# Kernel tuning notes

Measured on AMD Instinct MI355X. Metric: run time of the kernel, lower is better.

Reference implementation:

```python
import jax, jax.numpy as jnp
import numpy as np
from jax import lax


def _sobel3d_kernels():
    # Standard separable 3D Sobel: derivative d=[-1,0,1] along one axis,
    # smoothing s=[1,2,1] along the other two. Axes order (D, H, W).
    d = np.array([-1.0, 0.0, 1.0], dtype=np.float32)
    s = np.array([1.0, 2.0, 1.0], dtype=np.float32)
    kx = np.einsum('i,j,k->ijk', d, s, s)  # derivative along D
    ky = np.einsum('i,j,k->ijk', s, d, s)  # derivative along H
    kz = np.einsum('i,j,k->ijk', s, s, d)  # derivative along W
    # Stack as [Cout=3, Cin=1, 3, 3, 3] -> one conv computes x,y,z grads at once.
    return jnp.asarray(np.stack([kx, ky, kz])[:, None])


_DN = ('NCDHW', 'OIDHW', 'NCDHW')


def _conv3(x, k):
    # x: [N, 1, D, H, W], k: [3, 1, 3, 3, 3] -> [N, 3, D-2, H-2, W-2]
    # torch F.conv3d and lax conv are both cross-correlation; VALID padding.
    return lax.conv_general_dilated(x, k, (1, 1, 1), 'VALID', dimension_numbers=_DN)


def _g2(inp, k):
    # inp: [B, D, H, W, C] (channels last, as the torch module permutes)
    b, dd, hh, ww, c = inp.shape
    x = jnp.transpose(inp, (0, 4, 1, 2, 3)).reshape(b * c, 1, dd, hh, ww)
    g1 = _conv3(x, k)                                  # [B*C, 3, D-2, H-2, W-2]
    mag = jnp.sqrt(jnp.sum(g1 * g1, axis=1, keepdims=True))  # first-order magnitude
    g2 = _conv3(mag, k)                                # [B*C, 3, D-4, H-4, W-4]
    gx, gy, gz = g2[:, 0], g2[:, 1], g2[:, 2]
    # Faithful to source: sqrt(x^2 + y^2) + z^2 (note: z is squared, not inside sqrt)
    out = jnp.sqrt(gx * gx + gy * gy) + gz * gz        # [B*C, D-4, H-4, W-4]
    return out.reshape(b, c, *out.shape[1:])


def setup_inputs() -> dict:
    key = jax.random.key(0)
    k1, k2 = jax.random.split(key)
    pred = jax.random.normal(k1, (2, 64, 64, 64, 32), dtype=jnp.float32)
    hr = jax.random.normal(k2, (2, 64, 64, 64, 32), dtype=jnp.float32)
    return {'pred': pred, 'hr': hr}


def reference(pred, hr):
    k = _sobel3d_kernels()
    return jnp.mean(jnp.abs(_g2(pred, k) - _g2(hr, k)))
```

## Files before the change

kernel.cpp:

```cpp
#include <hip/hip_runtime.h>
#include <hip/hip_fp16.h>


constexpr int BDIM = 256;
constexpr size_t IN_B = 8388608;
constexpr int IN_D = 131072;
constexpr int IN_H = 2048;
constexpr int M = 62;
constexpr int F = 60;
constexpr int C = 32;
constexpr int MROW = M * C;
constexpr size_t MAGSZ = (size_t)M * M * MROW;
constexpr size_t PLANE = (size_t)M * MROW;
constexpr unsigned NPART = 1440;

__device__ __forceinline__ float4 ld4(const float* p) {
    return *reinterpret_cast<const float4*>(p);
}
__device__ __forceinline__ float4 ldh4(const __half* p) {
    float2 r = *reinterpret_cast<const float2*>(p);
    const __half2* h = reinterpret_cast<const __half2*>(&r);
    float2 lo = __half22float2(h[0]), hi = __half22float2(h[1]);
    return make_float4(lo.x, lo.y, hi.x, hi.y);
}
__device__ __forceinline__ float4 sm3(float4 a, float4 b, float4 c) {
    return make_float4(a.x + 2.f * b.x + c.x, a.y + 2.f * b.y + c.y,
                       a.z + 2.f * b.z + c.z, a.w + 2.f * b.w + c.w);
}
__device__ __forceinline__ float4 df2(float4 a, float4 c) {
    return make_float4(c.x - a.x, c.y - a.y, c.z - a.z, c.w - a.w);
}

struct P1W { float4 A[2], B[2], C[2]; };

__device__ __forceinline__ void p1_plane(const float* __restrict__ col, size_t zoff,
                                         P1W& W)
{
    float4 S[4], D[4];
#pragma unroll
    for (int r = 0; r < 4; ++r) {
        const float* p = col + zoff + (size_t)r * IN_H;
        float4 a = ld4(p), b = ld4(p + C), c = ld4(p + 2 * C);
        S[r] = sm3(a, b, c);
        D[r] = df2(a, c);
    }
#pragma unroll
    for (int k = 0; k < 2; ++k) {
        W.A[k] = sm3(S[k], S[k+1], S[k+2]);
        W.B[k] = df2(S[k], S[k+2]);
        W.C[k] = sm3(D[k], D[k+1], D[k+2]);
    }
}

__device__ __forceinline__ void p1_emit(const P1W& W0, const P1W& W1, const P1W& W2,
                                        __half* __restrict__ mag, size_t cb,
                                        int z, int y0, bool wr)
{
    if (!wr) return;
#pragma unroll
    for (int k = 0; k < 2; ++k) {
        float4 gx = df2(W0.A[k], W2.A[k]);
        float4 gy = sm3(W0.B[k], W1.B[k], W2.B[k]);
        float4 gz = sm3(W0.C[k], W1.C[k], W2.C[k]);
        float m0 = sqrtf(gx.x * gx.x + gy.x * gy.x + gz.x * gz.x);
        float m1 = sqrtf(gx.y * gx.y + gy.y * gy.y + gz.y * gz.y);
        float m2 = sqrtf(gx.z * gx.z + gy.z * gy.z + gz.z * gz.z);
        float m3 = sqrtf(gx.w * gx.w + gy.w * gy.w + gz.w * gz.w);
        union { __half2 h[2]; float2 f; } u;
        u.h[0] = __floats2half2_rn(m0, m1);
        u.h[1] = __floats2half2_rn(m2, m3);
        *reinterpret_cast<float2*>(mag + ((size_t)z * M + (y0 + k)) * MROW + cb)
            = u.f;
    }
}

__device__ __forceinline__ void p1_unit(const float* __restrict__ in,
                                        __half* __restrict__ mag,
                                        int b, int bx, int zc, int tid)
{
    const int xt = bx & 1, yt = bx >> 1;
    const int c4 = (tid & 7) << 2;
    const int xl = tid >> 3;
    const int x  = xt * 30 + xl;
    const bool wr = (xt == 0) || (xl >= 2);
    const int y0 = yt * 2;
    const int z0 = zc * 8;
    const int zn = min(8, M - z0);

    const float* col = in + (size_t)b * IN_B + (size_t)y0 * IN_H
                          + (size_t)x * C + c4;
    const size_t cb = (size_t)x * C + c4;

    P1W W0, W1, W2;
    p1_plane(col, (size_t)(z0 + 0) * IN_D, W0);
    p1_plane(col, (size_t)(z0 + 1) * IN_D, W1);
    int z = 0;
    while (true) {
        p1_plane(col, (size_t)(z0 + z + 2) * IN_D, W2);
        p1_emit(W0, W1, W2, mag, cb, z0 + z, y0, wr);
        if (++z >= zn) break;
        p1_plane(col, (size_t)(z0 + z + 2) * IN_D, W0);
        p1_emit(W1, W2, W0, mag, cb, z0 + z, y0, wr);
        if (++z >= zn) break;
        p1_plane(col, (size_t)(z0 + z + 2) * IN_D, W1);
        p1_emit(W2, W0, W1, mag, cb, z0 + z, y0, wr);
        if (++z >= zn) break;
    }
}

__global__ __launch_bounds__(BDIM) void sobel_mag_v10(
    const float* __restrict__ pred, const float* __restrict__ hr,
    __half* __restrict__ magP, __half* __restrict__ magH,
    int b, unsigned* __restrict__ counter, int zeroCtr)
{
    if (zeroCtr && blockIdx.x == 0 && blockIdx.y == 0 && blockIdx.z == 0 &&
        threadIdx.x == 0)
        __hip_atomic_store(counter, 0u, __ATOMIC_RELAXED,
                           __HIP_MEMORY_SCOPE_AGENT);
    const float* in = blockIdx.z ? hr : pred;
    __half* mag = blockIdx.z ? magH : magP;
    p1_unit(in, mag, b, blockIdx.x, blockIdx.y, threadIdx.x);
}

struct P2W4 { float4 A[2], B[2], C[2]; };

__device__ __forceinline__ void p2_plane4(const __half* __restrict__ col,
                                          size_t zoff, P2W4& W)
{
    float4 S[4], D[4];
#pragma unroll
    for (int r = 0; r < 4; ++r) {
        const __half* p = col + zoff + (size_t)r * MROW;
        float4 a = ldh4(p), b = ldh4(p + C), c = ldh4(p + 2 * C);
        S[r] = sm3(a, b, c);
        D[r] = df2(a, c);
    }
#pragma unroll
    for (int k = 0; k < 2; ++k) {
        W.A[k] = sm3(S[k], S[k+1], S[k+2]);
        W.B[k] = df2(S[k], S[k+2]);
        W.C[k] = sm3(D[k], D[k+1], D[k+2]);
    }
}

__device__ __forceinline__ void p2_emit4(const P2W4& P0, const P2W4& P1, const P2W4& P2,
                                         const P2W4& H0, const P2W4& H1, const P2W4& H2,
                                         float& acc)
{
#pragma unroll
    for (int k = 0; k < 2; ++k) {
        float4 gxP = df2(P0.A[k], P2.A[k]);
        float4 gyP = sm3(P0.B[k], P1.B[k], P2.B[k]);
        float4 gzP = sm3(P0.C[k], P1.C[k], P2.C[k]);
        float4 gxH = df2(H0.A[k], H2.A[k]);
        float4 gyH = sm3(H0.B[k], H1.B[k], H2.B[k]);
        float4 gzH = sm3(H0.C[k], H1.C[k], H2.C[k]);
        acc += fabsf((sqrtf(gxP.x*gxP.x + gyP.x*gyP.x) + gzP.x*gzP.x)
                   - (sqrtf(gxH.x*gxH.x + gyH.x*gyH.x) + gzH.x*gzH.x));
        acc += fabsf((sqrtf(gxP.y*gxP.y + gyP.y*gyP.y) + gzP.y*gzP.y)
                   - (sqrtf(gxH.y*gxH.y + gyH.y*gyH.y) + gzH.y*gzH.y));
        acc += fabsf((sqrtf(gxP.z*gxP.z + gyP.z*gyP.z) + gzP.z*gzP.z)
                   - (sqrtf(gxH.z*gxH.z + gyH.z*gyH.z) + gzH.z*gzH.z));
        acc += fabsf((sqrtf(gxP.w*gxP.w + gyP.w*gyP.w) + gzP.w*gzP.w)
                   - (sqrtf(gxH.w*gxH.w + gyH.w*gyH.w) + gzH.w*gzH.w));
    }
}

__global__ __launch_bounds__(BDIM) void sobel2_v10(
    const __half* __restrict__ magP, const __half* __restrict__ magH,
    int b, float* __restrict__ partial, unsigned* __restrict__ counter,
    float* __restrict__ out)
{
    const int bx = blockIdx.x;
    const int xt = bx & 1, yt = bx >> 1;
    const int zc = blockIdx.y;
    const int y0 = yt * 2;
    const int z0 = zc * 5;
    const int tid = threadIdx.x;
    const int c4 = (tid & 7) << 2;
    const int xl = tid >> 3;
    const bool wr = xl < 30;
    const int xo = xt * 30 + min(xl, 29);

    const size_t colo = (size_t)y0 * MROW + (size_t)xo * C + c4;
    const __half* colP = magP + colo;
    const __half* colH = magH + colo;

    P2W4 P0, P1, P2, H0, H1, H2;
    float acc = 0.f;
    p2_plane4(colP, (size_t)(z0 + 0) * PLANE, P0);
    p2_plane4(colH, (size_t)(z0 + 0) * PLANE, H0);
    p2_plane4(colP, (size_t)(z0 + 1) * PLANE, P1);
    p2_plane4(colH, (size_t)(z0 + 1) * PLANE, H1);

    p2_plane4(colP, (size_t)(z0 + 2) * PLANE, P2);
    p2_plane4(colH, (size_t)(z0 + 2) * PLANE, H2);
    if (wr) p2_emit4(P0, P1, P2, H0, H1, H2, acc);
    p2_plane4(colP, (size_t)(z0 + 3) * PLANE, P0);
    p2_plane4(colH, (size_t)(z0 + 3) * PLANE, H0);
    if (wr) p2_emit4(P1, P2, P0, H1, H2, H0, acc);
    p2_plane4(colP, (size_t)(z0 + 4) * PLANE, P1);
    p2_plane4(colH, (size_t)(z0 + 4) * PLANE, H1);
    if (wr) p2_emit4(P2, P0, P1, H2, H0, H1, acc);
    p2_plane4(colP, (size_t)(z0 + 5) * PLANE, P2);
    p2_plane4(colH, (size_t)(z0 + 5) * PLANE, H2);
    if (wr) p2_emit4(P0, P1, P2, H0, H1, H2, acc);
    p2_plane4(colP, (size_t)(z0 + 6) * PLANE, P0);
    p2_plane4(colH, (size_t)(z0 + 6) * PLANE, H0);
    if (wr) p2_emit4(P1, P2, P0, H1, H2, H0, acc);

    for (int o = 32; o > 0; o >>= 1) acc += __shfl_down(acc, o, 64);
    __shared__ float sred[BDIM / 64];
    __shared__ int isLast;
    __shared__ double sd[BDIM / 64];
    const int lane = tid & 63, wv = tid >> 6;
    if (lane == 0) sred[wv] = acc;
    __syncthreads();
    if (tid == 0) {
        float t = 0.f;
#pragma unroll
        for (int i = 0; i < BDIM / 64; ++i) t += sred[i];
        const size_t pidx = (size_t)b * 720 + (size_t)zc * 60 + bx;
        __hip_atomic_store(&partial[pidx], t, __ATOMIC_RELAXED,
                           __HIP_MEMORY_SCOPE_AGENT);
        const unsigned old = __hip_atomic_fetch_add(counter, 1u, __ATOMIC_ACQ_REL,
                                                    __HIP_MEMORY_SCOPE_AGENT);
        isLast = (old == NPART - 1u) ? 1 : 0;
    }
    __syncthreads();
    if (isLast) {
        double a = 0.0;
        for (unsigned i = tid; i < NPART; i += BDIM)
            a += (double)__hip_atomic_load(&partial[i], __ATOMIC_RELAXED,
                                           __HIP_MEMORY_SCOPE_AGENT);
        for (int o = 32; o > 0; o >>= 1) a += __shfl_down(a, o, 64);
        if (lane == 0) sd[wv] = a;
        __syncthreads();
        if (tid == 0) {
            double t = 0.0;
#pragma unroll
            for (int i = 0; i < BDIM / 64; ++i) t += sd[i];
            out[0] = (float)(t / 13824000.0);
        }
    }
}

extern "C" void kernel_launch(void* const* d_in, const int* in_sizes, int n_in,
                              void* d_out, int out_size, void* d_ws, size_t ws_size,
                              hipStream_t stream)
{
    const float* pred = (const float*)d_in[0];
    const float* hr   = (const float*)d_in[1];

    float* partial    = (float*)d_ws;
    unsigned* counter = (unsigned*)((char*)d_ws + 32768);
    __half* magP = (__half*)((char*)d_ws + 65536);
    __half* magH = magP + MAGSZ;

    for (int b = 0; b < 2; ++b) {
        sobel_mag_v10<<<dim3(62, 8, 2), BDIM, 0, stream>>>(
            pred, hr, magP, magH, b, counter, b == 0 ? 1 : 0);
        sobel2_v10<<<dim3(60, 12), BDIM, 0, stream>>>(
            magP, magH, b, partial, counter, (float*)d_out);
    }
}
```

Baseline: 268.1 us.

## Restructure second Sobel pass to 2-channel single-row threads with longer z-march

The second-stage kernel's per-thread work changes from four channels across two y-rows to two channels in one y-row, and each block now marches ten z-planes instead of five. The grid is rebuilt as 240×6 blocks, and the partial-sum indexing and NPART are resized to match. The aim is to lower register pressure, raise occupancy and cut wasted lanes, at the cost of less horizontal reuse between y-rows, since each thread reloads three rows for one output row, and a smaller vector load per thread.

```diff
diff --git a/kernel.cpp b/kernel.cpp
--- a/kernel.cpp
+++ b/kernel.cpp
@@ -12,16 +12,13 @@
 constexpr int MROW = M * C;
 constexpr size_t MAGSZ = (size_t)M * M * MROW;
 constexpr size_t PLANE = (size_t)M * MROW;
-constexpr unsigned NPART = 1440;
+constexpr unsigned NPART = 2880;
 
 __device__ __forceinline__ float4 ld4(const float* p) {
     return *reinterpret_cast<const float4*>(p);
 }
-__device__ __forceinline__ float4 ldh4(const __half* p) {
-    float2 r = *reinterpret_cast<const float2*>(p);
-    const __half2* h = reinterpret_cast<const __half2*>(&r);
-    float2 lo = __half22float2(h[0]), hi = __half22float2(h[1]);
-    return make_float4(lo.x, lo.y, hi.x, hi.y);
+__device__ __forceinline__ float2 ldh2(const __half* p) {
+    return __half22float2(*reinterpret_cast<const __half2*>(p));
 }
 __device__ __forceinline__ float4 sm3(float4 a, float4 b, float4 c) {
     return make_float4(a.x + 2.f * b.x + c.x, a.y + 2.f * b.y + c.y,
@@ -108,7 +105,7 @@
     }
 }
 
-__global__ __launch_bounds__(BDIM) void sobel_mag_v10(
+__global__ __launch_bounds__(BDIM) void sobel_mag_v11(
     const float* __restrict__ pred, const float* __restrict__ hr,
     __half* __restrict__ magP, __half* __restrict__ magH,
     int b, unsigned* __restrict__ counter, int zeroCtr)
@@ -122,92 +119,93 @@
     p1_unit(in, mag, b, blockIdx.x, blockIdx.y, threadIdx.x);
 }
 
-struct P2W4 { float4 A[2], B[2], C[2]; };
-
-__device__ __forceinline__ void p2_plane4(const __half* __restrict__ col,
-                                          size_t zoff, P2W4& W)
-{
-    float4 S[4], D[4];
-#pragma unroll
-    for (int r = 0; r < 4; ++r) {
-        const __half* p = col + zoff + (size_t)r * MROW;
-        float4 a = ldh4(p), b = ldh4(p + C), c = ldh4(p + 2 * C);
-        S[r] = sm3(a, b, c);
-        D[r] = df2(a, c);
-    }
-#pragma unroll
-    for (int k = 0; k < 2; ++k) {
-        W.A[k] = sm3(S[k], S[k+1], S[k+2]);
-        W.B[k] = df2(S[k], S[k+2]);
-        W.C[k] = sm3(D[k], D[k+1], D[k+2]);
-    }
-}
-
-__device__ __forceinline__ void p2_emit4(const P2W4& P0, const P2W4& P1, const P2W4& P2,
-                                         const P2W4& H0, const P2W4& H1, const P2W4& H2,
-                                         float& acc)
-{
-#pragma unroll
-    for (int k = 0; k < 2; ++k) {
-        float4 gxP = df2(P0.A[k], P2.A[k]);
-        float4 gyP = sm3(P0.B[k], P1.B[k], P2.B[k]);
-        float4 gzP = sm3(P0.C[k], P1.C[k], P2.C[k]);
-        float4 gxH = df2(H0.A[k], H2.A[k]);
-        float4 gyH = sm3(H0.B[k], H1.B[k], H2.B[k]);
-        float4 gzH = sm3(H0.C[k], H1.C[k], H2.C[k]);
-        acc += fabsf((sqrtf(gxP.x*gxP.x + gyP.x*gyP.x) + gzP.x*gzP.x)
-                   - (sqrtf(gxH.x*gxH.x + gyH.x*gyH.x) + gzH.x*gzH.x));
-        acc += fabsf((sqrtf(gxP.y*gxP.y + gyP.y*gyP.y) + gzP.y*gzP.y)
-                   - (sqrtf(gxH.y*gxH.y + gyH.y*gyH.y) + gzH.y*gzH.y));
-        acc += fabsf((sqrtf(gxP.z*gxP.z + gyP.z*gyP.z) + gzP.z*gzP.z)
-                   - (sqrtf(gxH.z*gxH.z + gyH.z*gyH.z) + gzH.z*gzH.z));
-        acc += fabsf((sqrtf(gxP.w*gxP.w + gyP.w*gyP.w) + gzP.w*gzP.w)
-                   - (sqrtf(gxH.w*gxH.w + gyH.w*gyH.w) + gzH.w*gzH.w));
-    }
-}
-
-__global__ __launch_bounds__(BDIM) void sobel2_v10(
+struct P2S { float2 A, B, C; };
+
+__device__ __forceinline__ void p2_plane_v11(const __half* __restrict__ col,
+                                             size_t zoff, P2S& W)
+{
+    float2 SX[3], DX[3];
+#pragma unroll
+    for (int j = 0; j < 3; ++j) {
+        const __half* p = col + zoff + (size_t)j * MROW;
+        float2 a = ldh2(p), b = ldh2(p + C), c = ldh2(p + 2 * C);
+        SX[j] = make_float2(a.x + 2.f * b.x + c.x, a.y + 2.f * b.y + c.y);
+        DX[j] = make_float2(c.x - a.x, c.y - a.y);
+    }
+    W.A = make_float2(SX[0].x + 2.f * SX[1].x + SX[2].x,
+                      SX[0].y + 2.f * SX[1].y + SX[2].y);
+    W.B = make_float2(SX[2].x - SX[0].x, SX[2].y - SX[0].y);
+    W.C = make_float2(DX[0].x + 2.f * DX[1].x + DX[2].x,
+                      DX[0].y + 2.f * DX[1].y + DX[2].y);
+}
+
+__device__ __forceinline__ void p2_emit_v11(const P2S& P0, const P2S& P1, const P2S& P2,
+                                            const P2S& H0, const P2S& H1, const P2S& H2,
+                                            float& acc)
+{
+    float gxPx = P2.A.x - P0.A.x;
+    float gxPy = P2.A.y - P0.A.y;
+    float gyPx = P0.B.x + 2.f * P1.B.x + P2.B.x;
+    float gyPy = P0.B.y + 2.f * P1.B.y + P2.B.y;
+    float gzPx = P0.C.x + 2.f * P1.C.x + P2.C.x;
+    float gzPy = P0.C.y + 2.f * P1.C.y + P2.C.y;
+    float gxHx = H2.A.x - H0.A.x;
+    float gxHy = H2.A.y - H0.A.y;
+    float gyHx = H0.B.x + 2.f * H1.B.x + H2.B.x;
+    float gyHy = H0.B.y + 2.f * H1.B.y + H2.B.y;
+    float gzHx = H0.C.x + 2.f * H1.C.x + H2.C.x;
+    float gzHy = H0.C.y + 2.f * H1.C.y + H2.C.y;
+    float oPx = sqrtf(gxPx * gxPx + gyPx * gyPx) + gzPx * gzPx;
+    float oPy = sqrtf(gxPy * gxPy + gyPy * gyPy) + gzPy * gzPy;
+    float oHx = sqrtf(gxHx * gxHx + gyHx * gyHx) + gzHx * gzHx;
+    float oHy = sqrtf(gxHy * gxHy + gyHy * gyHy) + gzHy * gzHy;
+    acc += fabsf(oPx - oHx) + fabsf(oPy - oHy);
+}
+
+__global__ __launch_bounds__(BDIM) void sobel2_v11(
     const __half* __restrict__ magP, const __half* __restrict__ magH,
     int b, float* __restrict__ partial, unsigned* __restrict__ counter,
     float* __restrict__ out)
 {
     const int bx = blockIdx.x;
-    const int xt = bx & 1, yt = bx >> 1;
+    const int xt = bx & 7, yt = bx >> 3;
     const int zc = blockIdx.y;
-    const int y0 = yt * 2;
-    const int z0 = zc * 5;
+    const int z0 = zc * 10;
     const int tid = threadIdx.x;
-    const int c4 = (tid & 7) << 2;
-    const int xl = tid >> 3;
-    const bool wr = xl < 30;
-    const int xo = xt * 30 + min(xl, 29);
-
-    const size_t colo = (size_t)y0 * MROW + (size_t)xo * C + c4;
+    const int yb = tid >> 7;
+    const int xl = (tid >> 4) & 7;
+    const int cp = tid & 15;
+    const int y  = yt * 2 + yb;
+    const int c2 = cp << 1;
+    const int xo = xt * 8 + xl;
+    const bool wr = xo < F;
+    const int xld = min(xo, F - 1);
+
+    const size_t colo = (size_t)y * MROW + (size_t)xld * C + c2;
     const __half* colP = magP + colo;
     const __half* colH = magH + colo;
 
-    P2W4 P0, P1, P2, H0, H1, H2;
+    P2S P0, P1, P2, H0, H1, H2;
     float acc = 0.f;
-    p2_plane4(colP, (size_t)(z0 + 0) * PLANE, P0);
-    p2_plane4(colH, (size_t)(z0 + 0) * PLANE, H0);
-    p2_plane4(colP, (size_t)(z0 + 1) * PLANE, P1);
-    p2_plane4(colH, (size_t)(z0 + 1) * PLANE, H1);
-
-    p2_plane4(colP, (size_t)(z0 + 2) * PLANE, P2);
-    p2_plane4(colH, (size_t)(z0 + 2) * PLANE, H2);
-    if (wr) p2_emit4(P0, P1, P2, H0, H1, H2, acc);
-    p2_plane4(colP, (size_t)(z0 + 3) * PLANE, P0);
-    p2_plane4(colH, (size_t)(z0 + 3) * PLANE, H0);
-    if (wr) p2_emit4(P1, P2, P0, H1, H2, H0, acc);
-    p2_plane4(colP, (size_t)(z0 + 4) * PLANE, P1);
-    p2_plane4(colH, (size_t)(z0 + 4) * PLANE, H1);
-    if (wr) p2_emit4(P2, P0, P1, H2, H0, H1, acc);
-    p2_plane4(colP, (size_t)(z0 + 5) * PLANE, P2);
-    p2_plane4(colH, (size_t)(z0 + 5) * PLANE, H2);
-    if (wr) p2_emit4(P0, P1, P2, H0, H1, H2, acc);
-    p2_plane4(colP, (size_t)(z0 + 6) * PLANE, P0);
-    p2_plane4(colH, (size_t)(z0 + 6) * PLANE, H0);
-    if (wr) p2_emit4(P1, P2, P0, H1, H2, H0, acc);
+    p2_plane_v11(colP, (size_t)(z0 + 0) * PLANE, P0);
+    p2_plane_v11(colH, (size_t)(z0 + 0) * PLANE, H0);
+    p2_plane_v11(colP, (size_t)(z0 + 1) * PLANE, P1);
+    p2_plane_v11(colH, (size_t)(z0 + 1) * PLANE, H1);
+    int z = 0;
+    while (true) {
+        p2_plane_v11(colP, (size_t)(z0 + z + 2) * PLANE, P2);
+        p2_plane_v11(colH, (size_t)(z0 + z + 2) * PLANE, H2);
+        if (wr) p2_emit_v11(P0, P1, P2, H0, H1, H2, acc);
+        if (++z >= 10) break;
+        p2_plane_v11(colP, (size_t)(z0 + z + 2) * PLANE, P0);
+        p2_plane_v11(colH, (size_t)(z0 + z + 2) * PLANE, H0);
+        if (wr) p2_emit_v11(P1, P2, P0, H1, H2, H0, acc);
+        if (++z >= 10) break;
+        p2_plane_v11(colP, (size_t)(z0 + z + 2) * PLANE, P1);
+        p2_plane_v11(colH, (size_t)(z0 + z + 2) * PLANE, H1);
+        if (wr) p2_emit_v11(P2, P0, P1, H2, H0, H1, acc);
+        if (++z >= 10) break;
+    }
 
     for (int o = 32; o > 0; o >>= 1) acc += __shfl_down(acc, o, 64);
     __shared__ float sred[BDIM / 64];
@@ -220,7 +218,7 @@
         float t = 0.f;
 #pragma unroll
         for (int i = 0; i < BDIM / 64; ++i) t += sred[i];
-        const size_t pidx = (size_t)b * 720 + (size_t)zc * 60 + bx;
+        const size_t pidx = (size_t)b * 1440 + (size_t)zc * 240 + bx;
         __hip_atomic_store(&partial[pidx], t, __ATOMIC_RELAXED,
                            __HIP_MEMORY_SCOPE_AGENT);
         const unsigned old = __hip_atomic_fetch_add(counter, 1u, __ATOMIC_ACQ_REL,
@@ -258,9 +256,9 @@
     __half* magH = magP + MAGSZ;
 
     for (int b = 0; b < 2; ++b) {
-        sobel_mag_v10<<<dim3(62, 8, 2), BDIM, 0, stream>>>(
+        sobel_mag_v11<<<dim3(62, 8, 2), BDIM, 0, stream>>>(
             pred, hr, magP, magH, b, counter, b == 0 ? 1 : 0);
-        sobel2_v10<<<dim3(60, 12), BDIM, 0, stream>>>(
+        sobel2_v11<<<dim3(240, 6), BDIM, 0, stream>>>(
             magP, magH, b, partial, counter, (float*)d_out);
     }
 }
```

Result: slower. 280.1 us (+4.5%).
